# Kernel tuning notes

Hardware: AMD Instinct MI355X
Metric: run time of the kernel (lower is better)

## Reference

```python
import jax, jax.numpy as jnp
import numpy as np

B, TOPN, OUT, PAD, IOU_TH, IM = 16, 4, 224, 224, 0.25, 448
HP = IM + 2 * PAD  # padded image side = 896

_ANCHOR_SETTINGS = (
    dict(stride=32, size=48, scale=[2 ** (1. / 3.), 2 ** (2. / 3.)], aspect_ratio=[0.667, 1, 1.5]),
    dict(stride=64, size=96, scale=[2 ** (1. / 3.), 2 ** (2. / 3.)], aspect_ratio=[0.667, 1, 1.5]),
    dict(stride=128, size=192, scale=[1, 2 ** (1. / 3.), 2 ** (2. / 3.)], aspect_ratio=[0.667, 1, 1.5]),
)

def _edge_anchors(input_shape=(IM, IM)):
    # NTS-Net generate_default_anchor_maps: per layer, loop scale then aspect,
    # each emitting an HxW map flattened row-major -> matches tidy conv channel-major flatten.
    out = []
    for a in _ANCHOR_SETTINGS:
        st = a['stride']
        H = int(np.ceil(input_shape[0] / st)); W = int(np.ceil(input_shape[1] / st))
        cy = np.broadcast_to((np.arange(H) * st + st / 2.)[:, None], (H, W))
        cx = np.broadcast_to((np.arange(W) * st + st / 2.)[None, :], (H, W))
        for sc in a['scale']:
            for ar in a['aspect_ratio']:
                h = a['size'] * sc / np.sqrt(ar); w = a['size'] * sc * np.sqrt(ar)
                out.append(np.stack([cy - h / 2., cx - w / 2., cy + h / 2., cx + w / 2.], -1).reshape(-1, 4))
    e = np.concatenate(out, 0)
    return (e + PAD).astype(np.int32)  # module does (edge_anchors + 224).astype(int)


def _conv(x, w, b, stride, pad):
    y = jax.lax.conv_general_dilated(x, w, (stride, stride), [(pad, pad), (pad, pad)],
                                     dimension_numbers=('NCHW', 'OIHW', 'NCHW'))
    return y + b[None, :, None, None]


def _proposal_scores(rpn, w1, b1, w2, b2, w3, b3, wt1, bt1, wt2, bt2, wt3, bt3):
    d1 = jax.nn.relu(_conv(rpn, w1, b1, 1, 1))   # [B,128,14,14]
    d2 = jax.nn.relu(_conv(d1, w2, b2, 2, 1))    # [B,128,7,7]
    d3 = jax.nn.relu(_conv(d2, w3, b3, 2, 1))    # [B,128,4,4]
    bsz = rpn.shape[0]
    t1 = _conv(d1, wt1, bt1, 1, 0).reshape(bsz, -1)  # [B,1176]
    t2 = _conv(d2, wt2, bt2, 1, 0).reshape(bsz, -1)  # [B,294]
    t3 = _conv(d3, wt3, bt3, 1, 0).reshape(bsz, -1)  # [B,144]
    return jnp.concatenate([t1, t2, t3], axis=1)     # [B,1614]


def _nms_topn(scores, boxes, areas):
    # greedy hard NMS, fixed TOPN picks, suppress iou >= IOU_TH (matches upstream hard_nms)
    def step(s, _):
        i = jnp.argmax(s)
        sb = boxes[i]
        iy = jnp.clip(jnp.minimum(boxes[:, 2], sb[2]) - jnp.maximum(boxes[:, 0], sb[0]), 0.)
        ix = jnp.clip(jnp.minimum(boxes[:, 3], sb[3]) - jnp.maximum(boxes[:, 1], sb[1]), 0.)
        inter = iy * ix
        iou = inter / (areas + areas[i] - inter)
        return jnp.where(iou >= IOU_TH, -jnp.inf, s), i
    _, idxs = jax.lax.scan(step, scores, None, length=TOPN)
    return idxs  # [TOPN] int


def _crop_resize(x, anchors, top_idx):
    # batched replacement of the per-(i,j) F.interpolate(x_pad[i,:,y0:y1,x0:x1], 224, bilinear, align_corners=True)
    x_pad = jnp.pad(x, ((0, 0), (0, 0), (PAD, PAD), (PAD, PAD)))
    xp = jnp.transpose(x_pad, (0, 2, 3, 1))            # [B,HP,HP,3]
    bxs = anchors[top_idx].astype(jnp.float32)          # [B,T,4] (y0,x0,y1,x1)
    y0, x0, y1, x1 = bxs[..., 0], bxs[..., 1], bxs[..., 2], bxs[..., 3]
    t = jnp.arange(OUT, dtype=jnp.float32) / (OUT - 1)  # align_corners=True grid
    ys = y0[..., None] + t * (y1 - y0 - 1.)[..., None]  # [B,T,S] src rows in padded img
    xs = x0[..., None] + t * (x1 - x0 - 1.)[..., None]
    yi0 = jnp.floor(ys).astype(jnp.int32); yi1 = jnp.minimum(yi0 + 1, HP - 1)
    xi0 = jnp.floor(xs).astype(jnp.int32); xi1 = jnp.minimum(xi0 + 1, HP - 1)
    wy = (ys - yi0)[..., :, None, None]                 # [B,T,S,1,1]
    wx = (xs - xi0)[..., None, :, None]                 # [B,T,1,S,1]
    b = jnp.arange(x.shape[0])[:, None, None, None]
    g = lambda yi, xi: xp[b, yi[..., :, None], xi[..., None, :]]  # [B,T,S,S,3]
    v = (g(yi0, xi0) * (1 - wy) * (1 - wx) + g(yi0, xi1) * (1 - wy) * wx
         + g(yi1, xi0) * wy * (1 - wx) + g(yi1, xi1) * wy * wx)
    return jnp.transpose(v, (0, 1, 4, 2, 3))            # [B,T,3,S,S]


def setup_inputs() -> dict:
    key = jax.random.key(0)
    ks = jax.random.split(key, 16)
    he = lambda k, shape, fan: jax.random.normal(k, shape, jnp.float32) * np.sqrt(2.0 / fan)
    inp = {
        'x': jax.random.normal(ks[0], (B, 3, IM, IM), jnp.float32),
        'rpn_feature': jax.random.uniform(ks[1], (B, 2048, 14, 14), jnp.float32),
        'w_down1': he(ks[2], (128, 2048, 3, 3), 2048 * 9), 'b_down1': jnp.zeros((128,), jnp.float32),
        'w_down2': he(ks[3], (128, 128, 3, 3), 128 * 9),   'b_down2': jnp.zeros((128,), jnp.float32),
        'w_down3': he(ks[4], (128, 128, 3, 3), 128 * 9),   'b_down3': jnp.zeros((128,), jnp.float32),
        'w_tidy1': he(ks[5], (6, 128, 1, 1), 128),         'b_tidy1': jnp.zeros((6,), jnp.float32),
        'w_tidy2': he(ks[6], (6, 128, 1, 1), 128),         'b_tidy2': jnp.zeros((6,), jnp.float32),
        'w_tidy3': he(ks[7], (9, 128, 1, 1), 128),         'b_tidy3': jnp.zeros((9,), jnp.float32),
        'anchors': jnp.asarray(_edge_anchors(), jnp.int32),  # [1614,4]
    }
    return inp


def reference(x, rpn_feature, w_down1, b_down1, w_down2, b_down2, w_down3, b_down3,
              w_tidy1, b_tidy1, w_tidy2, b_tidy2, w_tidy3, b_tidy3, anchors):
    rpn_score = _proposal_scores(rpn_feature, w_down1, b_down1, w_down2, b_down2, w_down3, b_down3,
                                 w_tidy1, b_tidy1, w_tidy2, b_tidy2, w_tidy3, b_tidy3)
    boxes = anchors.astype(jnp.float32)
    areas = (boxes[:, 2] - boxes[:, 0]) * (boxes[:, 3] - boxes[:, 1])
    top_idx = jax.vmap(lambda s: _nms_topn(s, boxes, areas))(rpn_score)       # [B,TOPN]
    top_prob = jnp.take_along_axis(rpn_score, top_idx, axis=1)                # [B,TOPN]
    part_imgs = _crop_resize(x, anchors, top_idx).reshape(B * TOPN, 3, OUT, OUT)
    return part_imgs, top_idx, top_prob, rpn_score
```

## Files before the change

kernel.cpp:

```cpp
#include <hip/hip_runtime.h>
#include <math.h>

#define BATCH 16
#define TOPN 4
#define OUTS 224
#define PADW 224
#define IM 448
#define HP 896
#define NA 1614
#define IC1 2048
#define C128 128

#define N_PART (BATCH*TOPN*3*OUTS*OUTS)
#define OFF_TOPIDX  (N_PART)
#define OFF_TOPPROB (N_PART + BATCH*TOPN)
#define OFF_SCORE   (N_PART + 2*BATCH*TOPN)

#define WS_D1 0
#define WS_IDX (BATCH*C128*196)
#define WS_WT  (WS_IDX + 64)
#define NWT1 (9*2048*128)
#define NWT2 (9*128*128)
#define NIMG (16*32*16384)

typedef __attribute__((ext_vector_type(8))) short frag8;
typedef __attribute__((ext_vector_type(16))) float acc16;
typedef __attribute__((ext_vector_type(4)))  float acc4;

__device__ __forceinline__ unsigned short f2bf(float f) {
    unsigned int u = __float_as_uint(f);
    u = (u + 0x7fffu + ((u >> 16) & 1u)) >> 16;
    return (unsigned short)u;
}
__device__ __forceinline__ float bf2f(unsigned short h) {
    return __uint_as_float(((unsigned int)h) << 16);
}
__device__ __forceinline__ void cvt4(const float* v, ushort4* h, ushort4* lo) {
    unsigned short hh[4], ll[4];
#pragma unroll
    for (int e = 0; e < 4; ++e) { hh[e] = f2bf(v[e]); ll[e] = f2bf(v[e] - bf2f(hh[e])); }
    *h  = make_ushort4(hh[0], hh[1], hh[2], hh[3]);
    *lo = make_ushort4(ll[0], ll[1], ll[2], ll[3]);
}

__device__ __forceinline__ void w1frag_body(const float* __restrict__ w1,
                                            unsigned short* __restrict__ w1h,
                                            unsigned short* __restrict__ w1l,
                                            int i) {
    if (i >= 32768) return;
    int oc5 = i & 31;
    int q8  = (i >> 5) & 1;
    int ot  = (i >> 6) & 3;
    int c   = (i >> 8) & 3;
    int h   = (i >> 10) & 1;
    int kg  = (i >> 11) & 15;
    int oc  = ot * 32 + oc5;
    int ic0 = kg * 128 + h * 64 + c * 16 + q8 * 8;
    int l   = q8 * 32 + oc5;
    const float* src = w1 + ((size_t)oc * IC1 + ic0) * 9;
    size_t dbase = (size_t)kg * 16384 + h * 8192 + c * 2048 + ot * 512 + l * 8;
#pragma unroll
    for (int t = 0; t < 9; ++t) {
        frag8 hv, lv;
#pragma unroll
        for (int e = 0; e < 8; ++e) {
            float v = src[e * 9 + t];
            unsigned short hs = f2bf(v);
            hv[e] = (short)hs;
            lv[e] = (short)f2bf(v - bf2f(hs));
        }
        size_t dst = dbase + (size_t)t * 262144;
        *(frag8*)&w1h[dst] = hv;
        *(frag8*)&w1l[dst] = lv;
    }
}

__device__ __forceinline__ void wfrag128_body(const float* __restrict__ w,
                                              unsigned short* __restrict__ wh,
                                              unsigned short* __restrict__ wl,
                                              int i) {
    if (i >= 16384) return;
    int oc5 = i & 31;
    int q8  = (i >> 5) & 1;
    int ot  = (i >> 6) & 3;
    int c   = (i >> 8) & 3;
    int h   = (i >> 10) & 1;
    int oc  = ot * 32 + oc5;
    int ic0 = h * 64 + c * 16 + q8 * 8;
    int l   = q8 * 32 + oc5;
    const float* src = w + ((size_t)oc * C128 + ic0) * 9;
    size_t dbase = (size_t)h * 8192 + c * 2048 + ot * 512 + l * 8;
#pragma unroll
    for (int t = 0; t < 9; ++t) {
        frag8 hv, lv;
#pragma unroll
        for (int e = 0; e < 8; ++e) {
            float v = src[e * 9 + t];
            unsigned short hs = f2bf(v);
            hv[e] = (short)hs;
            lv[e] = (short)f2bf(v - bf2f(hs));
        }
        size_t dst = dbase + (size_t)t * 16384;
        *(frag8*)&wh[dst] = hv;
        *(frag8*)&wl[dst] = lv;
    }
}

__global__ __launch_bounds__(256) void k_prep(
    const float* __restrict__ w1, unsigned short* __restrict__ w1h, unsigned short* __restrict__ w1l,
    const float* __restrict__ w2, unsigned short* __restrict__ w2fh, unsigned short* __restrict__ w2fl,
    const float* __restrict__ w3, unsigned short* __restrict__ w3fh, unsigned short* __restrict__ w3fl,
    const float* __restrict__ rpn, unsigned short* __restrict__ imgH,
    const float* __restrict__ b1, float* __restrict__ d1) {
    __shared__ float tile[64 * 201];
    const int tid = threadIdx.x;
    const int blk = blockIdx.x;
    if (blk < 128) {
        w1frag_body(w1, w1h, w1l, blk * 256 + tid);
    } else if (blk < 192) {
        wfrag128_body(w2, w2fh, w2fl, (blk - 128) * 256 + tid);
    } else if (blk < 256) {
        wfrag128_body(w3, w3fh, w3fl, (blk - 192) * 256 + tid);
    } else if (blk < 768) {
        const int bb = blk - 256;
        const int b = bb & 15, icg = bb >> 4;
        const int ic0 = icg * 64;
        char* img = (char*)(imgH + (size_t)bb * 16384);
        for (int qq = tid; qq < 3136; qq += 256) {
            int icl = qq / 49, r = qq % 49, p = r * 4;
            const float4 v = *(const float4*)&rpn[(size_t)(b * IC1 + ic0 + icl) * 196 + p];
            tile[icl * 201 + p + 0] = v.x;
            tile[icl * 201 + p + 1] = v.y;
            tile[icl * 201 + p + 2] = v.z;
            tile[icl * 201 + p + 3] = v.w;
        }
        __syncthreads();
        for (int qq = tid; qq < 3136; qq += 256) {
            int px = qq >> 4, ic4 = (qq & 15) * 4;
            float vv[4];
            unsigned short hh[4];
#pragma unroll
            for (int e = 0; e < 4; ++e) { vv[e] = tile[(ic4 + e) * 201 + px]; hh[e] = f2bf(vv[e]); }
            int pos = (px / 14 + 1) * 16 + (px % 14 + 1);
            int byo = (pos * 128 + ic4 * 2) ^ ((pos & 7) << 4);
            *(ushort4*)(img + byo) = make_ushort4(hh[0], hh[1], hh[2], hh[3]);
        }
        for (int qq = tid; qq < 960; qq += 256) {
            int hp = qq >> 4, sub = qq & 15;
            int pos;
            if (hp < 16)      pos = hp;
            else if (hp < 32) pos = 240 + (hp - 16);
            else if (hp < 46) pos = (hp - 31) * 16;
            else              pos = (hp - 45) * 16 + 15;
            *(ushort4*)(img + pos * 128 + sub * 8) = make_ushort4(0, 0, 0, 0);
        }
    } else {
        int i = (blk - 768) * 256 + tid;
        int base = i * 4;
        float4 v;
        v.x = b1[(base + 0) & 127]; v.y = b1[(base + 1) & 127];
        v.z = b1[(base + 2) & 127]; v.w = b1[(base + 3) & 127];
        *(float4*)&d1[base] = v;
    }
}


#define LOADB(it, BH, BL) { \
    const int o_ = ((it) >> 2) * 262144 + ((it) & 3) * 2048; \
    BH = *(const frag8*)&WHb[o_]; BL = *(const frag8*)&WLb[o_]; }

#define DOMFMA(it, BH, BL) { \
    const int tap_ = (it) >> 2; \
    const int off_ = (tap_ / 3) * 16 + (tap_ % 3); \
    const int kb_ = ((it) & 3) * 32 + q * 16; \
    frag8 aH[4]; \
    _Pragma("unroll") \
    for (int mt_ = 0; mt_ < 4; ++mt_) { \
        const int p_ = posa[mt_] + off_; \
        const int by_ = (p_ * 128 + kb_) ^ ((p_ & 7) << 4); \
        aH[mt_] = *(const frag8*)((const char*)inH + by_); \
    } \
    _Pragma("unroll") \
    for (int mt_ = 0; mt_ < 4; ++mt_) { \
        acc[mt_] = __builtin_amdgcn_mfma_f32_32x32x16_bf16(aH[mt_], BH, acc[mt_], 0, 0, 0); \
        acc[mt_] = __builtin_amdgcn_mfma_f32_32x32x16_bf16(aH[mt_], BL, acc[mt_], 0, 0, 0); \
    } }

__global__ __launch_bounds__(512, 4) void k_conv1_mfma(const unsigned short* __restrict__ imgH,
                                                       const unsigned short* __restrict__ wfh,
                                                       const unsigned short* __restrict__ wfl,
                                                       float* __restrict__ d1) {
    __shared__ unsigned short inH[256 * 64];

    const int tid = threadIdx.x;
    const int blk = blockIdx.x;
    const int b = blk >> 5;
    const int icg = blk & 31;
    const int l = tid & 63, w = tid >> 6;
    const int ln = l & 31, q = l >> 5;
    const int mtw = w & 1, ntw = w >> 1;

    {
        const char* src = (const char*)(imgH + ((size_t)(icg * 16 + b)) * 16384);
        char* dst = (char*)inH;
#pragma unroll
        for (int k = 0; k < 4; ++k) {
            frag8 v = *(const frag8*)(src + tid * 16 + k * 8192);
            *(frag8*)(dst + tid * 16 + k * 8192) = v;
        }
    }

    acc16 acc[4];
#pragma unroll
    for (int mt = 0; mt < 4; ++mt)
#pragma unroll
        for (int r = 0; r < 16; ++r) acc[mt][r] = 0.f;

    int posa[4];
#pragma unroll
    for (int mt = 0; mt < 4; ++mt) {
        int px = mtw * 128 + mt * 32 + ln;
        posa[mt] = (px < 196) ? ((px / 14) * 16 + (px % 14)) : 0;
    }

    const unsigned short* WHb = wfh + (size_t)icg * 8192 + ntw * 512 + (size_t)l * 8;
    const unsigned short* WLb = wfl + (size_t)icg * 8192 + ntw * 512 + (size_t)l * 8;

    __syncthreads();

    frag8 B0H, B0L, B1H, B1L, B2H, B2L;
    LOADB(0, B0H, B0L);
    LOADB(1, B1H, B1L);
    LOADB(2, B2H, B2L);
#pragma unroll
    for (int g = 0; g < 12; ++g) {
        DOMFMA(g * 3 + 0, B0H, B0L); if (g < 11) LOADB(g * 3 + 3, B0H, B0L);
        DOMFMA(g * 3 + 1, B1H, B1L); if (g < 11) LOADB(g * 3 + 4, B1H, B1L);
        DOMFMA(g * 3 + 2, B2H, B2L); if (g < 11) LOADB(g * 3 + 5, B2H, B2L);
    }

    {
        const int oc = ntw * 32 + ln;
#pragma unroll
        for (int mt = 0; mt < 4; ++mt) {
#pragma unroll
            for (int r = 0; r < 16; ++r) {
                int m = (r & 3) + 8 * (r >> 2) + 4 * q;
                int px = mtw * 128 + mt * 32 + m;
                if (px < 196)
                    atomicAdd(&d1[(size_t)(b * 196 + px) * 128 + oc], acc[mt][r]);
            }
        }
    }
}


#define LOADB2(it, BH, BL) { \
    const int o_ = ((it) >> 2) * 16384 + ((it) & 3) * 2048; \
    BH = *(const frag8*)&W2H[o_]; BL = *(const frag8*)&W2L[o_]; }

#define DOC2(it, BH, BL) { \
    const int tap_ = (it) >> 2; \
    const int off_ = (tap_ / 3) * 16 + (tap_ % 3); \
    const int ko_ = ((it) & 3) * 16 + q * 8; \
    const int pp_ = (posa2 + off_) * 72 + ko_; \
    frag8 aH = *(const frag8*)&inH[pp_]; \
    frag8 aL = *(const frag8*)&inL[pp_]; \
    c2 = __builtin_amdgcn_mfma_f32_32x32x16_bf16(aH, BH, c2, 0, 0, 0); \
    c2 = __builtin_amdgcn_mfma_f32_32x32x16_bf16(aH, BL, c2, 0, 0, 0); \
    c2 = __builtin_amdgcn_mfma_f32_32x32x16_bf16(aL, BH, c2, 0, 0, 0); }

#define LOADB3(it, BH, BL) { \
    const int o_ = ((it) >> 2) * 16384 + ((it) & 3) * 2048; \
    BH = *(const frag8*)&W3Hp[o_]; BL = *(const frag8*)&W3Lp[o_]; }

#define DOC3(it, BH, BL) { \
    const int tap_ = (it) >> 2; \
    const int off_ = (tap_ / 3) * 16 + (tap_ % 3); \
    const int ko_ = ((it) & 3) * 16 + q * 8; \
    const int pp_ = (posb3 + off_) * 72 + ko_; \
    frag8 aH = *(const frag8*)&dhH[pp_]; \
    frag8 aL = *(const frag8*)&dhL[pp_]; \
    c3 = __builtin_amdgcn_mfma_f32_32x32x16_bf16(aH, BH, c3, 0, 0, 0); \
    c3 = __builtin_amdgcn_mfma_f32_32x32x16_bf16(aH, BL, c3, 0, 0, 0); \
    c3 = __builtin_amdgcn_mfma_f32_32x32x16_bf16(aL, BH, c3, 0, 0, 0); }

__global__ __launch_bounds__(512, 1) void k_tail(
    const float* __restrict__ d1,
    const unsigned short* __restrict__ w2fh, const unsigned short* __restrict__ w2fl,
    const unsigned short* __restrict__ w3fh, const unsigned short* __restrict__ w3fl,
    const float* __restrict__ b2, const float* __restrict__ b3,
    const float* __restrict__ wt1, const float* __restrict__ bt1,
    const float* __restrict__ wt2, const float* __restrict__ bt2,
    const float* __restrict__ wt3, const float* __restrict__ bt3,
    const int* __restrict__ anchors,
    float* __restrict__ score_out, float* __restrict__ out_idx,
    float* __restrict__ out_prob, int* __restrict__ idx_ws) {
    extern __shared__ char smem[];
    unsigned short* inH = (unsigned short*)(smem);
    unsigned short* inL = (unsigned short*)(smem + 43776);
    unsigned short* t1H = (unsigned short*)(smem + 124416);
    unsigned short* t1L = (unsigned short*)(smem + 126720);
    float*  d2f  = (float*)(smem + 129024);
    float*  sbuf = (float*)(smem + 154112);
    unsigned short* dhH = (unsigned short*)(smem);
    unsigned short* dhL = (unsigned short*)(smem + 27648);
    float*  d3f  = (float*)(smem + 55296);
    unsigned short* t2H = (unsigned short*)(smem + 63488);
    unsigned short* t2L = (unsigned short*)(smem + 65792);
    float* wt3s = (float*)(smem);
    float* y0s = (float*)(smem + 6464);
    float* x0s = (float*)(smem + 12928);
    float* y1s = (float*)(smem + 19392);
    float* x1s = (float*)(smem + 25856);
    float* ars = (float*)(smem + 32320);
    float* rv  = (float*)(smem + 38784);
    int*   ri  = (int*)(smem + 39808);

    const int tid = threadIdx.x;
    const int b = blockIdx.x;
    const int l = tid & 63, w = tid >> 6;
    const int ln = l & 31, q = l >> 5;
    const int l16 = l & 15, q4 = l >> 4;

    for (int i = tid; i < 304 * 72; i += 512) { inH[i] = 0; inL[i] = 0; }

    acc16 c2;
    acc4 t1a[2];
#pragma unroll
    for (int r = 0; r < 16; ++r) c2[r] = 0.f;
#pragma unroll
    for (int i = 0; i < 2; ++i)
#pragma unroll
        for (int r = 0; r < 4; ++r) t1a[i][r] = 0.f;

    const int mtw = w & 1, ntw = w >> 1;
    int posa2;
    {
        int px = mtw * 32 + ln;
        posa2 = (px < 49) ? ((px / 7) * 32 + (px % 7) * 2) : 256;
    }
    __syncthreads();

    for (int half = 0; half < 2; ++half) {
        const int ics = half * 64;
        for (int qq = tid; qq < 3136; qq += 512) {
            int px = qq >> 4, ic4 = (qq & 15) * 4;
            float4 v = *(const float4*)&d1[(size_t)(b * 196 + px) * 128 + ics + ic4];
            float vv[4] = {fmaxf(v.x, 0.f), fmaxf(v.y, 0.f), fmaxf(v.z, 0.f), fmaxf(v.w, 0.f)};
            ushort4 h4, l4; cvt4(vv, &h4, &l4);
            int pos = (px / 14 + 1) * 16 + (px % 14 + 1);
            *(ushort4*)&inH[pos * 72 + ic4] = h4;
            *(ushort4*)&inL[pos * 72 + ic4] = l4;
        }
        for (int qq = tid; qq < 1024; qq += 512) {
            int m = qq >> 6, k = qq & 63;
            float v = (m < 6) ? wt1[m * 128 + ics + k] : 0.f;
            unsigned short h = f2bf(v);
            t1H[m * 72 + k] = h;
            t1L[m * 72 + k] = f2bf(v - bf2f(h));
        }
        __syncthreads();

        {
            const unsigned short* W2H = w2fh + half * 8192 + ntw * 512 + (size_t)l * 8;
            const unsigned short* W2L = w2fl + half * 8192 + ntw * 512 + (size_t)l * 8;
            frag8 B0H, B0L, B1H, B1L, B2H, B2L, B3H, B3L;
            LOADB2(0, B0H, B0L);
            LOADB2(1, B1H, B1L);
            LOADB2(2, B2H, B2L);
            LOADB2(3, B3H, B3L);
#pragma unroll
            for (int g = 0; g < 9; ++g) {
                DOC2(g * 4 + 0, B0H, B0L); if (g < 8) LOADB2(g * 4 + 4, B0H, B0L);
                DOC2(g * 4 + 1, B1H, B1L); if (g < 8) LOADB2(g * 4 + 5, B1H, B1L);
                DOC2(g * 4 + 2, B2H, B2L); if (g < 8) LOADB2(g * 4 + 6, B2H, B2L);
                DOC2(g * 4 + 3, B3H, B3L); if (g < 8) LOADB2(g * 4 + 7, B3H, B3L);
            }
        }

#pragma unroll
        for (int i = 0; i < 2; ++i) {
            int px = (w * 2 + i) * 16 + l16;
            int pos = (px < 196) ? ((px / 14 + 1) * 16 + (px % 14 + 1)) : 256;
#pragma unroll
            for (int c = 0; c < 2; ++c) {
                int ko = c * 32 + q4 * 8;
                frag8 aH = *(const frag8*)&t1H[l16 * 72 + ko];
                frag8 aL = *(const frag8*)&t1L[l16 * 72 + ko];
                frag8 bH = *(const frag8*)&inH[pos * 72 + ko];
                frag8 bL = *(const frag8*)&inL[pos * 72 + ko];
                t1a[i] = __builtin_amdgcn_mfma_f32_16x16x32_bf16(aH, bH, t1a[i], 0, 0, 0);
                t1a[i] = __builtin_amdgcn_mfma_f32_16x16x32_bf16(aH, bL, t1a[i], 0, 0, 0);
                t1a[i] = __builtin_amdgcn_mfma_f32_16x16x32_bf16(aL, bH, t1a[i], 0, 0, 0);
            }
        }
        __syncthreads();
    }

    {
        int oc = ntw * 32 + ln;
        float bias = b2[oc];
#pragma unroll
        for (int r = 0; r < 16; ++r) {
            int m = (r & 3) + 8 * (r >> 2) + 4 * q;
            int px = mtw * 32 + m;
            if (px < 49) d2f[px * 128 + oc] = fmaxf(c2[r] + bias, 0.f);
        }
    }
#pragma unroll
    for (int i = 0; i < 2; ++i) {
        int px = (w * 2 + i) * 16 + l16;
#pragma unroll
        for (int r = 0; r < 4; ++r) {
            int oc = q4 * 4 + r;
            if (oc < 6 && px < 196) {
                float v = t1a[i][r] + bt1[oc];
                sbuf[oc * 196 + px] = v;
                score_out[b * NA + oc * 196 + px] = v;
            }
        }
    }
    __syncthreads();

    for (int i = tid; i < 192 * 72; i += 512) { dhH[i] = 0; dhL[i] = 0; }

    acc16 c3;
    acc4 t2a;
#pragma unroll
    for (int r = 0; r < 16; ++r) c3[r] = 0.f;
#pragma unroll
    for (int r = 0; r < 4; ++r) t2a[r] = 0.f;

    const int posb3 = (ln < 16) ? ((ln / 4) * 32 + (ln % 4) * 2) : 144;
    const int pxt2 = (w - 4) * 16 + l16;
    const int posbt2 = (w >= 4 && pxt2 < 49) ? ((pxt2 / 7 + 1) * 16 + (pxt2 % 7 + 1)) : 144;
    __syncthreads();

    for (int half = 0; half < 2; ++half) {
        const int ics = half * 64;
        for (int qq = tid; qq < 784; qq += 512) {
            int px = qq >> 4, ic4 = (qq & 15) * 4;
            float4 v = *(const float4*)&d2f[px * 128 + ics + ic4];
            float vv[4] = {v.x, v.y, v.z, v.w};
            ushort4 h4, l4; cvt4(vv, &h4, &l4);
            int pos = (px / 7 + 1) * 16 + (px % 7 + 1);
            *(ushort4*)&dhH[pos * 72 + ic4] = h4;
            *(ushort4*)&dhL[pos * 72 + ic4] = l4;
        }
        for (int qq = tid; qq < 1024; qq += 512) {
            int m = qq >> 6, k = qq & 63;
            float v = (m < 6) ? wt2[m * 128 + ics + k] : 0.f;
            unsigned short h = f2bf(v);
            t2H[m * 72 + k] = h;
            t2L[m * 72 + k] = f2bf(v - bf2f(h));
        }
        __syncthreads();

        if (w < 4) {
            const unsigned short* W3Hp = w3fh + half * 8192 + w * 512 + (size_t)l * 8;
            const unsigned short* W3Lp = w3fl + half * 8192 + w * 512 + (size_t)l * 8;
            frag8 B0H, B0L, B1H, B1L, B2H, B2L, B3H, B3L;
            LOADB3(0, B0H, B0L);
            LOADB3(1, B1H, B1L);
            LOADB3(2, B2H, B2L);
            LOADB3(3, B3H, B3L);
#pragma unroll
            for (int g = 0; g < 9; ++g) {
                DOC3(g * 4 + 0, B0H, B0L); if (g < 8) LOADB3(g * 4 + 4, B0H, B0L);
                DOC3(g * 4 + 1, B1H, B1L); if (g < 8) LOADB3(g * 4 + 5, B1H, B1L);
                DOC3(g * 4 + 2, B2H, B2L); if (g < 8) LOADB3(g * 4 + 6, B2H, B2L);
                DOC3(g * 4 + 3, B3H, B3L); if (g < 8) LOADB3(g * 4 + 7, B3H, B3L);
            }
        } else {
#pragma unroll
            for (int c = 0; c < 2; ++c) {
                int ko = c * 32 + q4 * 8;
                frag8 aH = *(const frag8*)&t2H[l16 * 72 + ko];
                frag8 aL = *(const frag8*)&t2L[l16 * 72 + ko];
                frag8 bH = *(const frag8*)&dhH[posbt2 * 72 + ko];
                frag8 bL = *(const frag8*)&dhL[posbt2 * 72 + ko];
                t2a = __builtin_amdgcn_mfma_f32_16x16x32_bf16(aH, bH, t2a, 0, 0, 0);
                t2a = __builtin_amdgcn_mfma_f32_16x16x32_bf16(aH, bL, t2a, 0, 0, 0);
                t2a = __builtin_amdgcn_mfma_f32_16x16x32_bf16(aL, bH, t2a, 0, 0, 0);
            }
        }
        __syncthreads();
    }

    if (w < 4) {
        int oc = w * 32 + ln;
        float bias = b3[oc];
#pragma unroll
        for (int r = 0; r < 16; ++r) {
            int px = (r & 3) + 8 * (r >> 2) + 4 * q;
            if (px < 16) d3f[oc * 16 + px] = fmaxf(c3[r] + bias, 0.f);
        }
    } else {
#pragma unroll
        for (int r = 0; r < 4; ++r) {
            int oc = q4 * 4 + r;
            if (oc < 6 && pxt2 < 49) {
                float v = t2a[r] + bt2[oc];
                sbuf[1176 + oc * 49 + pxt2] = v;
                score_out[b * NA + 1176 + oc * 49 + pxt2] = v;
            }
        }
    }
    for (int i = tid; i < 1152; i += 512) wt3s[i] = wt3[i];
    __syncthreads();

    if (tid < 144) {
        int oc = tid >> 4, px = tid & 15;
        float s = bt3[oc];
        for (int ic = 0; ic < 128; ++ic) s += wt3s[oc * 128 + ic] * d3f[ic * 16 + px];
        sbuf[1470 + oc * 16 + px] = s;
        score_out[b * NA + 1470 + oc * 16 + px] = s;
    }
    for (int j = tid; j < NA; j += 512) {
        int4 a = ((const int4*)anchors)[j];
        float a0 = (float)a.x, a1 = (float)a.y, a2 = (float)a.z, a3 = (float)a.w;
        y0s[j] = a0; x0s[j] = a1; y1s[j] = a2; x1s[j] = a3;
        ars[j] = (a2 - a0) * (a3 - a1);
    }
    __syncthreads();

    for (int it = 0; it < TOPN; ++it) {
        float bv = -INFINITY; int bi = NA;
        for (int j = tid; j < NA; j += 512) {
            float v = sbuf[j];
            if (v > bv || (v == bv && j < bi)) { bv = v; bi = j; }
        }
#pragma unroll
        for (int d = 1; d < 64; d <<= 1) {
            float ov = __shfl_xor(bv, d, 64);
            int   oi = __shfl_xor(bi, d, 64);
            if (ov > bv || (ov == bv && oi < bi)) { bv = ov; bi = oi; }
        }
        if (l == 0) { rv[w] = bv; ri[w] = bi; }
        __syncthreads();
        if (tid == 0) {
            float V = rv[0]; int K = ri[0];
#pragma unroll
            for (int j = 1; j < 8; ++j) {
                float ov = rv[j]; int oi = ri[j];
                if (ov > V || (ov == V && oi < K)) { V = ov; K = oi; }
            }
            ri[8] = K;
            out_idx[b * TOPN + it] = (float)K;
            out_prob[b * TOPN + it] = V;
            idx_ws[b * TOPN + it] = K;
        }
        __syncthreads();
        int K = ri[8];
        float ky0 = y0s[K], kx0 = x0s[K], ky1 = y1s[K], kx1 = x1s[K], ka = ars[K];
        for (int j = tid; j < NA; j += 512) {
            float iy = fmaxf(fminf(y1s[j], ky1) - fmaxf(y0s[j], ky0), 0.f);
            float ix = fmaxf(fminf(x1s[j], kx1) - fmaxf(x0s[j], kx0), 0.f);
            float inter = iy * ix;
            float iou = inter / (ars[j] + ka - inter);
            if (iou >= 0.25f) sbuf[j] = -INFINITY;
        }
        __syncthreads();
    }
}

__global__ __launch_bounds__(256) void k_crop(const float* __restrict__ x,
                                              const int* __restrict__ anchors,
                                              const int* __restrict__ idx_ws,
                                              float* __restrict__ out) {
    int blk = blockIdx.x;
    int crop = blk / OUTS;
    int i = blk % OUTS;
    int j = threadIdx.x;
    if (j >= OUTS) return;
    int b = crop >> 2;
    int a = idx_ws[crop];
    int y0 = anchors[a * 4], x0 = anchors[a * 4 + 1];
    int y1 = anchors[a * 4 + 2], x1 = anchors[a * 4 + 3];

    float ti = (float)i / 223.f;
    float ys = (float)y0 + ti * (float)(y1 - y0 - 1);
    int yi0 = (int)ys;
    int yi1 = min(yi0 + 1, HP - 1);
    float wy = ys - (float)yi0;

    float tj = (float)j / 223.f;
    float xs = (float)x0 + tj * (float)(x1 - x0 - 1);
    int xi0 = (int)xs;
    int xi1 = min(xi0 + 1, HP - 1);
    float wx = xs - (float)xi0;

    int ry0 = yi0 - PADW, ry1 = yi1 - PADW, rx0 = xi0 - PADW, rx1 = xi1 - PADW;
    bool vy0 = (ry0 >= 0) && (ry0 < IM), vy1 = (ry1 >= 0) && (ry1 < IM);
    bool vx0 = (rx0 >= 0) && (rx0 < IM), vx1 = (rx1 >= 0) && (rx1 < IM);

    float w00 = (1.f - wy) * (1.f - wx), w01 = (1.f - wy) * wx;
    float w10 = wy * (1.f - wx), w11 = wy * wx;

#pragma unroll
    for (int c = 0; c < 3; ++c) {
        const float* xp = x + (size_t)(b * 3 + c) * IM * IM;
        float g00 = (vy0 && vx0) ? xp[ry0 * IM + rx0] : 0.f;
        float g01 = (vy0 && vx1) ? xp[ry0 * IM + rx1] : 0.f;
        float g10 = (vy1 && vx0) ? xp[ry1 * IM + rx0] : 0.f;
        float g11 = (vy1 && vx1) ? xp[ry1 * IM + rx1] : 0.f;
        out[(size_t)(crop * 3 + c) * OUTS * OUTS + i * OUTS + j] =
            g00 * w00 + g01 * w01 + g10 * w10 + g11 * w11;
    }
}

extern "C" void kernel_launch(void* const* d_in, const int* in_sizes, int n_in,
                              void* d_out, int out_size, void* d_ws, size_t ws_size,
                              hipStream_t stream) {
    (void)in_sizes; (void)n_in; (void)out_size; (void)ws_size;
    const float* x    = (const float*)d_in[0];
    const float* rpn  = (const float*)d_in[1];
    const float* w1   = (const float*)d_in[2];
    const float* b1   = (const float*)d_in[3];
    const float* w2   = (const float*)d_in[4];
    const float* b2   = (const float*)d_in[5];
    const float* w3   = (const float*)d_in[6];
    const float* b3   = (const float*)d_in[7];
    const float* wt1  = (const float*)d_in[8];
    const float* bt1  = (const float*)d_in[9];
    const float* wt2  = (const float*)d_in[10];
    const float* bt2  = (const float*)d_in[11];
    const float* wt3  = (const float*)d_in[12];
    const float* bt3  = (const float*)d_in[13];
    const int*   anc  = (const int*)d_in[14];

    float* out = (float*)d_out;
    float* ws  = (float*)d_ws;
    float* d1  = ws + WS_D1;
    int*   idxw = (int*)(ws + WS_IDX);
    unsigned short* w1h = (unsigned short*)(ws + WS_WT);
    unsigned short* w1l = w1h + NWT1;
    unsigned short* w2fh = w1l + NWT1;
    unsigned short* w2fl = w2fh + NWT2;
    unsigned short* w3fh = w2fl + NWT2;
    unsigned short* w3fl = w3fh + NWT2;
    unsigned short* imgH = w3fl + NWT2;

    static const int TAIL_LDS = 160568;
    hipFuncSetAttribute((const void*)k_tail, hipFuncAttributeMaxDynamicSharedMemorySize, TAIL_LDS);

    k_prep<<<1160, 256, 0, stream>>>(w1, w1h, w1l, w2, w2fh, w2fl, w3, w3fh, w3fl,
                                     rpn, imgH, b1, d1);
    k_conv1_mfma<<<512, 512, 0, stream>>>(imgH, w1h, w1l, d1);
    k_tail<<<BATCH, 512, TAIL_LDS, stream>>>(d1, w2fh, w2fl, w3fh, w3fl, b2, b3,
                                             wt1, bt1, wt2, bt2, wt3, bt3, anc,
                                             out + OFF_SCORE, out + OFF_TOPIDX,
                                             out + OFF_TOPPROB, idxw);
    k_crop<<<BATCH * TOPN * OUTS, 256, 0, stream>>>(x, anc, idxw, out);
}
```

Measured before the change: 272.3 us.

## Replace split-K atomicAdd with per-block partial buffers and a reduce kernel

```diff
diff --git a/kernel.cpp b/kernel.cpp
--- a/kernel.cpp
+++ b/kernel.cpp
@@ -22,6 +22,7 @@
 #define NWT1 (9*2048*128)
 #define NWT2 (9*128*128)
 #define NIMG (16*32*16384)
+#define D1SL 25088
 
 typedef __attribute__((ext_vector_type(8))) short frag8;
 typedef __attribute__((ext_vector_type(16))) float acc16;
@@ -110,8 +111,7 @@
     const float* __restrict__ w1, unsigned short* __restrict__ w1h, unsigned short* __restrict__ w1l,
     const float* __restrict__ w2, unsigned short* __restrict__ w2fh, unsigned short* __restrict__ w2fl,
     const float* __restrict__ w3, unsigned short* __restrict__ w3fh, unsigned short* __restrict__ w3fl,
-    const float* __restrict__ rpn, unsigned short* __restrict__ imgH,
-    const float* __restrict__ b1, float* __restrict__ d1) {
+    const float* __restrict__ rpn, unsigned short* __restrict__ imgH) {
     __shared__ float tile[64 * 201];
     const int tid = threadIdx.x;
     const int blk = blockIdx.x;
@@ -121,7 +121,7 @@
         wfrag128_body(w2, w2fh, w2fl, (blk - 128) * 256 + tid);
     } else if (blk < 256) {
         wfrag128_body(w3, w3fh, w3fl, (blk - 192) * 256 + tid);
-    } else if (blk < 768) {
+    } else {
         const int bb = blk - 256;
         const int b = bb & 15, icg = bb >> 4;
         const int ic0 = icg * 64;
@@ -154,13 +154,6 @@
             else              pos = (hp - 45) * 16 + 15;
             *(ushort4*)(img + pos * 128 + sub * 8) = make_ushort4(0, 0, 0, 0);
         }
-    } else {
-        int i = (blk - 768) * 256 + tid;
-        int base = i * 4;
-        float4 v;
-        v.x = b1[(base + 0) & 127]; v.y = b1[(base + 1) & 127];
-        v.z = b1[(base + 2) & 127]; v.w = b1[(base + 3) & 127];
-        *(float4*)&d1[base] = v;
     }
 }
 
@@ -189,7 +182,7 @@
 __global__ __launch_bounds__(512, 4) void k_conv1_mfma(const unsigned short* __restrict__ imgH,
                                                        const unsigned short* __restrict__ wfh,
                                                        const unsigned short* __restrict__ wfl,
-                                                       float* __restrict__ d1) {
+                                                       float* __restrict__ d1p) {
     __shared__ unsigned short inH[256 * 64];
 
     const int tid = threadIdx.x;
@@ -240,6 +233,7 @@
     }
 
     {
+        float* out = d1p + (size_t)blk * D1SL;
         const int oc = ntw * 32 + ln;
 #pragma unroll
         for (int mt = 0; mt < 4; ++mt) {
@@ -248,10 +242,29 @@
                 int m = (r & 3) + 8 * (r >> 2) + 4 * q;
                 int px = mtw * 128 + mt * 32 + m;
                 if (px < 196)
-                    atomicAdd(&d1[(size_t)(b * 196 + px) * 128 + oc], acc[mt][r]);
-            }
-        }
-    }
+                    out[px * 128 + oc] = acc[mt][r];
+            }
+        }
+    }
+}
+
+__global__ __launch_bounds__(256) void k_reduce(const float* __restrict__ d1p,
+                                                const float* __restrict__ b1,
+                                                float* __restrict__ d1) {
+    int f4 = blockIdx.x * 256 + threadIdx.x;
+    int flat = f4 * 4;
+    int b = flat / D1SL;
+    int inner = flat - b * D1SL;
+    const float* src = d1p + (size_t)b * 32 * D1SL + inner;
+    float4 s = *(const float4*)&b1[inner & 127];
+#pragma unroll 8
+    for (int icg = 0; icg < 32; ++icg) {
+        float4 v = *(const float4*)&src[(size_t)icg * D1SL];
+        s.x += v.x; s.y += v.y; s.z += v.z; s.w += v.w;
+    }
+    s.x = fmaxf(s.x, 0.f); s.y = fmaxf(s.y, 0.f);
+    s.z = fmaxf(s.z, 0.f); s.w = fmaxf(s.w, 0.f);
+    *(float4*)&d1[flat] = s;
 }
 
 
@@ -641,13 +654,15 @@
     unsigned short* w3fh = w2fl + NWT2;
     unsigned short* w3fl = w3fh + NWT2;
     unsigned short* imgH = w3fl + NWT2;
+    float* d1p = (float*)(imgH + NIMG);
 
     static const int TAIL_LDS = 160568;
     hipFuncSetAttribute((const void*)k_tail, hipFuncAttributeMaxDynamicSharedMemorySize, TAIL_LDS);
 
-    k_prep<<<1160, 256, 0, stream>>>(w1, w1h, w1l, w2, w2fh, w2fl, w3, w3fh, w3fl,
-                                     rpn, imgH, b1, d1);
-    k_conv1_mfma<<<512, 512, 0, stream>>>(imgH, w1h, w1l, d1);
+    k_prep<<<768, 256, 0, stream>>>(w1, w1h, w1l, w2, w2fh, w2fl, w3, w3fh, w3fl,
+                                    rpn, imgH);
+    k_conv1_mfma<<<512, 512, 0, stream>>>(imgH, w1h, w1l, d1p);
+    k_reduce<<<392, 256, 0, stream>>>(d1p, b1, d1);
     k_tail<<<BATCH, 512, TAIL_LDS, stream>>>(d1, w2fh, w2fl, w3fh, w3fl, b2, b3,
                                              wt1, bt1, wt2, bt2, wt3, bt3, anc,
                                              out + OFF_SCORE, out + OFF_TOPIDX,
```

After: 261.8 us. -3.9%, faster.
